# Kernel tuning notes

Hardware: AMD Instinct MI355X
Metric: run time of the kernel (lower is better)

## Reference

```python
import jax, jax.numpy as jnp
import numpy as np

B, C_IN, C_MID, C_OUT, R, K = 2048, 64, 64, 128, 60, 13
EPS = 1e-5


def _gather(x, nei):
    # x: [B, C, 60] -> gather neighbors -> [B, C, 60, 13]
    b, c = x.shape[0], x.shape[1]
    return x[:, :, nei].reshape(b, c, R, K)


def _block(x, nei, g, bta, m, v, W, c):
    # BN (eval mode) -> ReLU -> Conv2d(kernel (1,13)) fused block.
    h = _gather(x, nei)                              # [B,C,60,13]
    inv = g * jax.lax.rsqrt(v + EPS)                 # [C]
    h = jax.nn.relu(h * inv[None, :, None, None] + (bta - m * inv)[None, :, None, None])
    # Conv2d with kernel (1,13), stride 1 == contraction over (c, k)
    return jnp.einsum('bcrk,ock->bor', h, W) + c[None, :, None]  # [B,O,60]


def setup_inputs() -> dict:
    key = jax.random.key(0)
    ks = jax.random.split(key, 24)
    n = lambda k, s: jax.random.normal(k, s, dtype=jnp.float32)
    u = lambda k, s: jax.random.uniform(k, s, dtype=jnp.float32, minval=0.5, maxval=1.5)
    return {
        "x": n(ks[0], (B, C_IN, R)),
        "nei": jax.random.randint(ks[1], (R * K,), 0, R, dtype=jnp.int32),
        # comb_layer_in: BN(in) + Conv(in->mid)
        "g1": n(ks[2], (C_IN,)), "b1": n(ks[3], (C_IN,)), "m1": n(ks[4], (C_IN,)), "v1": u(ks[5], (C_IN,)),
        "W1": n(ks[6], (C_MID, C_IN, K)) * 0.1, "c1": n(ks[7], (C_MID,)) * 0.1,
        # comb_layer_out: BN(mid) + Conv(mid->out)
        "g2": n(ks[8], (C_MID,)), "b2": n(ks[9], (C_MID,)), "m2": n(ks[10], (C_MID,)), "v2": u(ks[11], (C_MID,)),
        "W2": n(ks[12], (C_OUT, C_MID, K)) * 0.1, "c2": n(ks[13], (C_OUT,)) * 0.1,
        # short_cut_layer: BN(in) + Conv(in->out)
        "g3": n(ks[14], (C_IN,)), "b3": n(ks[15], (C_IN,)), "m3": n(ks[16], (C_IN,)), "v3": u(ks[17], (C_IN,)),
        "W3": n(ks[18], (C_OUT, C_IN, K)) * 0.1, "c3": n(ks[19], (C_OUT,)) * 0.1,
    }


def reference(x, nei, g1, b1, m1, v1, W1, c1, g2, b2, m2, v2, W2, c2,
              g3, b3, m3, v3, W3, c3):
    f = _block(x, nei, g1, b1, m1, v1, W1, c1)      # [B, C_MID, 60]
    f = _block(f, nei, g2, b2, m2, v2, W2, c2)      # [B, C_OUT, 60]
    sc = _block(x, nei, g3, b3, m3, v3, W3, c3)     # [B, C_OUT, 60]
    return f + sc
```

## Files before the change

kernel.cpp:

```cpp
#include <hip/hip_runtime.h>
#include <hip/hip_bf16.h>


typedef __attribute__((ext_vector_type(8))) short bf16x8;
typedef __attribute__((ext_vector_type(4))) float f32x4;
typedef __attribute__((ext_vector_type(4))) unsigned short us4;
typedef __attribute__((ext_vector_type(8))) unsigned short us8;

#define EPSV 1e-5f
#define PLANE 131072
#define ZTOT  7864320

__device__ __forceinline__ unsigned short f2bf(float f) {
  unsigned int u = __builtin_bit_cast(unsigned int, f);
  u += 0x7FFFu + ((u >> 16) & 1u);
  return (unsigned short)(u >> 16);
}
__device__ __forceinline__ float bf2f(unsigned short s) {
  unsigned int u = ((unsigned int)s) << 16;
  return __builtin_bit_cast(float, u);
}

typedef const __attribute__((address_space(1))) unsigned int gas_u32;
typedef __attribute__((address_space(3))) unsigned int las_u32;
__device__ __forceinline__ void gl16(const void* g, void* l) {
  __builtin_amdgcn_global_load_lds((gas_u32*)g, (las_u32*)l, 16, 0, 0);
}

__global__ void prep_w(const float* __restrict__ W1, const float* __restrict__ W2,
                       const float* __restrict__ W3,
                       const float* __restrict__ g1, const float* __restrict__ be1,
                       const float* __restrict__ mu1, const float* __restrict__ va1,
                       const float* __restrict__ c1,
                       const float* __restrict__ g2, const float* __restrict__ be2,
                       const float* __restrict__ mu2, const float* __restrict__ va2,
                       const float* __restrict__ c2,
                       const float* __restrict__ g3, const float* __restrict__ be3,
                       const float* __restrict__ mu3, const float* __restrict__ va3,
                       const float* __restrict__ c3,
                       unsigned short* __restrict__ W1t,
                       unsigned short* __restrict__ W23t,
                       float* __restrict__ params) {
  int t = blockIdx.x * 256 + threadIdx.x;
  if (t < 4096) {
    int o = t >> 6, c = t & 63;
    const float* src = W1 + (o * 64 + c) * 13;
    unsigned short* dst = W1t + o * 832 + c;
    #pragma unroll
    for (int ks = 0; ks < 13; ks++) dst[ks * 64] = f2bf(src[ks]);
  } else if (t < 20480) {
    int idx = t - 4096;
    int half = idx >> 13;
    int o = (idx >> 6) & 127, c = idx & 63;
    const float* src = (half ? W3 : W2) + (o * 64 + c) * 13;
    unsigned short* dst = W23t + o * 1664 + half * 13 * 64 + c;
    #pragma unroll
    for (int ks = 0; ks < 13; ks++) dst[ks * 64] = f2bf(src[ks]);
  }
  if (blockIdx.x == 79) {
    int u = threadIdx.x;
    if (u < 64) {
      float a1v = g1[u] * rsqrtf(va1[u] + EPSV);
      params[u]       = a1v;
      params[64 + u]  = be1[u] - mu1[u] * a1v;
      float a3v = g3[u] * rsqrtf(va3[u] + EPSV);
      params[128 + u] = a3v;
      params[192 + u] = be3[u] - mu3[u] * a3v;
      float a2v = g2[u] * rsqrtf(va2[u] + EPSV);
      params[256 + u] = a2v;
      params[320 + u] = be2[u] - mu2[u] * a2v + a2v * c1[u];
    }
    if (u < 128) params[384 + u] = c2[u] + c3[u];
  }
}

__global__ __launch_bounds__(256) void t_in(const float* __restrict__ x,
                                            const float* __restrict__ params,
                                            unsigned short* __restrict__ z1T,
                                            unsigned short* __restrict__ z3T) {
  __shared__ float xt[64 * 61];
  __shared__ float prm[256];
  const int b = blockIdx.x, t = threadIdx.x;
  prm[t] = params[t];
  for (int i = t; i < 3840; i += 256) {
    int c = i / 60;
    xt[c * 61 + (i - c * 60)] = x[b * 3840 + i];
  }
  __syncthreads();
  if (t < 240) {
    int r = t >> 2, g = t & 3, c0 = g << 4;
    us8 z1v0, z1v1, z3v0, z3v1;
    #pragma unroll
    for (int j = 0; j < 8; j++) {
      int c = c0 + j;
      float v = xt[c * 61 + r];
      z1v0[j] = f2bf(fmaxf(fmaf(v, prm[c], prm[64 + c]), 0.f));
      z3v0[j] = f2bf(fmaxf(fmaf(v, prm[128 + c], prm[192 + c]), 0.f));
    }
    #pragma unroll
    for (int j = 0; j < 8; j++) {
      int c = c0 + 8 + j;
      float v = xt[c * 61 + r];
      z1v1[j] = f2bf(fmaxf(fmaf(v, prm[c], prm[64 + c]), 0.f));
      z3v1[j] = f2bf(fmaxf(fmaf(v, prm[128 + c], prm[192 + c]), 0.f));
    }
    int idx = (r * 2048 + b) * 64 + c0;
    *(us8*)(z1T + idx) = z1v0;  *(us8*)(z1T + idx + 8) = z1v1;
    *(us8*)(z3T + idx) = z3v0;  *(us8*)(z3T + idx + 8) = z3v1;
  }
}

#define MFMA __builtin_amdgcn_mfma_f32_16x16x32_bf16

__global__ __launch_bounds__(256, 2) void gemm1(const unsigned short* __restrict__ W1t,
                                                const unsigned short* __restrict__ z1T,
                                                const int* __restrict__ nei,
                                                const float* __restrict__ params,
                                                unsigned short* __restrict__ z2T) {
  __shared__ unsigned short As[2][4096];
  __shared__ unsigned short Bs[2][2][8192];

  const int bid = blockIdx.x;
  const int rp = bid >> 4, btile = bid & 15;
  const int b0 = btile << 7;
  const int rA = rp * 2, rB = rA + 1;
  const int t = threadIdx.x, wave = t >> 6, lane = t & 63;
  const int quad = lane >> 4, nl = lane & 15;
  const int rsel = wave >> 1, nhh = wave & 1;

  int pl0[13], pl1[13];
  #pragma unroll
  for (int q = 0; q < 13; q++) { pl0[q] = nei[rA * 13 + q]; pl1[q] = nei[rB * 13 + q]; }

  const int trow = t >> 3, tj = t & 7;
  const int sw8 = ((tj ^ (trow & 7)) << 3);
  const unsigned short* gA = W1t + trow * 832 + tj * 8;
  const unsigned short* gB = z1T + (b0 + trow) * 64 + tj * 8;
  unsigned short* lA = &As[0][trow * 64 + sw8];
  unsigned short* lB0 = &Bs[0][0][trow * 64 + sw8];
  unsigned short* lB1 = &Bs[0][1][trow * 64 + sw8];

  {
    us8 va0 = *(const us8*)(gA);
    us8 va1 = *(const us8*)(gA + 32 * 832);
    const unsigned short* g0 = gB + pl0[0] * PLANE;
    const unsigned short* g1p = gB + pl1[0] * PLANE;
    us8 b00 = *(const us8*)(g0);
    us8 b01 = *(const us8*)(g0 + 2048);
    us8 b02 = *(const us8*)(g0 + 4096);
    us8 b03 = *(const us8*)(g0 + 6144);
    us8 b10 = *(const us8*)(g1p);
    us8 b11 = *(const us8*)(g1p + 2048);
    us8 b12 = *(const us8*)(g1p + 4096);
    us8 b13 = *(const us8*)(g1p + 6144);
    *(us8*)(lA) = va0;  *(us8*)(lA + 2048) = va1;
    *(us8*)(lB0) = b00; *(us8*)(lB0 + 2048) = b01;
    *(us8*)(lB0 + 4096) = b02; *(us8*)(lB0 + 6144) = b03;
    *(us8*)(lB1) = b10; *(us8*)(lB1 + 2048) = b11;
    *(us8*)(lB1 + 4096) = b12; *(us8*)(lB1 + 6144) = b13;
  }
  __syncthreads();

  const int c0 = ((quad ^ (nl & 7)) << 3);
  f32x4 acc[4][4] = {};
  #pragma unroll 1
  for (int kq = 0; kq < 13; kq++) {
    const int bf = kq & 1;
    us8 va0, va1, b00, b01, b02, b03, b10, b11, b12, b13;
    if (kq < 12) {
      const unsigned short* ga = gA + (kq + 1) * 64;
      va0 = *(const us8*)(ga);
      va1 = *(const us8*)(ga + 32 * 832);
      const unsigned short* g0 = gB + pl0[kq + 1] * PLANE;
      const unsigned short* g1p = gB + pl1[kq + 1] * PLANE;
      b00 = *(const us8*)(g0);        b01 = *(const us8*)(g0 + 2048);
      b02 = *(const us8*)(g0 + 4096); b03 = *(const us8*)(g0 + 6144);
      b10 = *(const us8*)(g1p);        b11 = *(const us8*)(g1p + 2048);
      b12 = *(const us8*)(g1p + 4096); b13 = *(const us8*)(g1p + 6144);
    }
    const unsigned short* Ab = &As[bf][nl * 64];
    const unsigned short* Bb = &Bs[bf][rsel][(nhh * 64 + nl) * 64];
    bf16x8 af[4][2], bfr[4][2];
    #pragma unroll
    for (int mt = 0; mt < 4; mt++) {
      af[mt][0] = *(const bf16x8*)(Ab + mt * 1024 + c0);
      af[mt][1] = *(const bf16x8*)(Ab + mt * 1024 + (c0 ^ 32));
    }
    #pragma unroll
    for (int nt = 0; nt < 4; nt++) {
      bfr[nt][0] = *(const bf16x8*)(Bb + nt * 1024 + c0);
      bfr[nt][1] = *(const bf16x8*)(Bb + nt * 1024 + (c0 ^ 32));
    }
    #pragma unroll
    for (int h = 0; h < 2; h++)
      #pragma unroll
      for (int mt = 0; mt < 4; mt++)
        #pragma unroll
        for (int nt = 0; nt < 4; nt++)
          acc[mt][nt] = MFMA(af[mt][h], bfr[nt][h], acc[mt][nt], 0, 0, 0);
    if (kq < 12) {
      unsigned short* la = lA + (bf ^ 1) * 4096;
      unsigned short* l0 = lB0 + (bf ^ 1) * 16384;
      unsigned short* l1 = lB1 + (bf ^ 1) * 16384;
      *(us8*)(la) = va0;  *(us8*)(la + 2048) = va1;
      *(us8*)(l0) = b00; *(us8*)(l0 + 2048) = b01;
      *(us8*)(l0 + 4096) = b02; *(us8*)(l0 + 6144) = b03;
      *(us8*)(l1) = b10; *(us8*)(l1 + 2048) = b11;
      *(us8*)(l1 + 4096) = b12; *(us8*)(l1 + 6144) = b13;
    }
    __syncthreads();
  }

  const int rr = rA + rsel;
  #pragma unroll
  for (int mt = 0; mt < 4; mt++) {
    int ob = mt * 16 + quad * 4;
    f32x4 av = *(const f32x4*)(params + 256 + ob);
    f32x4 bv = *(const f32x4*)(params + 320 + ob);
    #pragma unroll
    for (int nt = 0; nt < 4; nt++) {
      int col = b0 + nhh * 64 + nt * 16 + nl;
      f32x4 a = acc[mt][nt];
      us4 w;
      w.x = f2bf(fmaxf(fmaf(a[0], av[0], bv[0]), 0.f));
      w.y = f2bf(fmaxf(fmaf(a[1], av[1], bv[1]), 0.f));
      w.z = f2bf(fmaxf(fmaf(a[2], av[2], bv[2]), 0.f));
      w.w = f2bf(fmaxf(fmaf(a[3], av[3], bv[3]), 0.f));
      *(us4*)(z2T + (rr * 2048 + col) * 64 + ob) = w;
    }
  }
}

__global__ __launch_bounds__(256, 2) void gemm2(const unsigned short* __restrict__ W23t,
                                                const unsigned short* __restrict__ z2T,
                                                const unsigned short* __restrict__ z3T,
                                                const int* __restrict__ nei,
                                                const float* __restrict__ params,
                                                unsigned short* __restrict__ outT) {
  __shared__ unsigned short As[3][4096];
  __shared__ unsigned short Bs[3][8192];
  __shared__ int sOff[26];

  const int bid = blockIdx.x;
  const int r = bid >> 3, btile = bid & 7;
  const int b0 = btile << 8;
  const int t = threadIdx.x, wv = t >> 6, lane = t & 63;
  const int quad = lane >> 4, nl = lane & 15;
  const int mh = wv >> 1, nh = wv & 1;

  if (t < 26) {
    int idx = t < 13 ? t : t - 13;
    int p = nei[r * 13 + idx];
    sOff[t] = p * (PLANE * 2) + (t < 13 ? 0 : ZTOT * 2);
  }

  const int lr = lane >> 2, lj = lane & 3;
  const int sj = ((lj ^ ((lr >> 1) & 3)) << 4);
  int aoff[2];
  #pragma unroll
  for (int i = 0; i < 2; i++) aoff[i] = (16 * (2 * wv + i) + lr) * 3328 + sj;
  int boff[4];
  #pragma unroll
  for (int i = 0; i < 4; i++) boff[i] = (b0 + 16 * (4 * wv + i) + lr) * 128 + sj;

  const char* gAb = (const char*)W23t;
  const char* z2b = (const char*)z2T;

  __syncthreads();

  {
    const char* gb = z2b + sOff[0];
    #pragma unroll
    for (int i = 0; i < 2; i++) gl16(gAb + aoff[i], &As[0][(2 * wv + i) * 512]);
    #pragma unroll
    for (int i = 0; i < 4; i++) gl16(gb + boff[i], &Bs[0][(4 * wv + i) * 512]);
    #pragma unroll
    for (int i = 0; i < 2; i++) gl16(gAb + 64 + aoff[i], &As[1][(2 * wv + i) * 512]);
    #pragma unroll
    for (int i = 0; i < 4; i++) gl16(gb + 64 + boff[i], &Bs[1][(4 * wv + i) * 512]);
  }
  asm volatile("s_waitcnt vmcnt(6)" ::: "memory");
  __builtin_amdgcn_s_barrier();

  const int rc = ((quad ^ ((nl >> 1) & 3)) << 3);
  const int aro = (mh * 64 + nl) * 32 + rc;
  const int bro = (nh * 128 + nl) * 32 + rc;

  f32x4 acc[4][8] = {};
  int cb = 0, sb = 2;
  #pragma unroll 1
  for (int s = 0; s < 51; s++) {
    const unsigned short* Ab = &As[cb][aro];
    const unsigned short* Bb = &Bs[cb][bro];
    bf16x8 af[4], bfr[8];
    #pragma unroll
    for (int mt = 0; mt < 4; mt++)
      af[mt] = *(const bf16x8*)(Ab + mt * 512);
    #pragma unroll
    for (int nt = 0; nt < 8; nt++)
      bfr[nt] = *(const bf16x8*)(Bb + nt * 512);
    const int kn = s + 2;
    if (kn < 52) {
      const int pn = kn >> 1;
      int off = sOff[pn] + ((kn & 1) << 6);
      const char* ga = gAb + kn * 64;
      const char* gb = z2b + off;
      #pragma unroll
      for (int i = 0; i < 2; i++) gl16(ga + aoff[i], &As[sb][(2 * wv + i) * 512]);
      #pragma unroll
      for (int i = 0; i < 4; i++) gl16(gb + boff[i], &Bs[sb][(4 * wv + i) * 512]);
    }
    __builtin_amdgcn_s_barrier();
    asm volatile("s_waitcnt lgkmcnt(0)" ::: "memory");
    __builtin_amdgcn_sched_barrier(0);
    __builtin_amdgcn_s_setprio(1);
    #pragma unroll
    for (int mt = 0; mt < 4; mt++)
      #pragma unroll
      for (int nt = 0; nt < 8; nt++)
        acc[mt][nt] = MFMA(af[mt], bfr[nt], acc[mt][nt], 0, 0, 0);
    __builtin_amdgcn_s_setprio(0);
    __builtin_amdgcn_sched_barrier(0);
    asm volatile("s_waitcnt vmcnt(6)" ::: "memory");
    __builtin_amdgcn_s_barrier();
    cb = (cb == 2) ? 0 : cb + 1;
    sb = (sb == 2) ? 0 : sb + 1;
  }
  {
    asm volatile("s_waitcnt vmcnt(0)" ::: "memory");
    __builtin_amdgcn_s_barrier();
    const unsigned short* Ab = &As[0][aro];
    const unsigned short* Bb = &Bs[0][bro];
    bf16x8 af[4], bfr[8];
    #pragma unroll
    for (int mt = 0; mt < 4; mt++)
      af[mt] = *(const bf16x8*)(Ab + mt * 512);
    #pragma unroll
    for (int nt = 0; nt < 8; nt++)
      bfr[nt] = *(const bf16x8*)(Bb + nt * 512);
    #pragma unroll
    for (int mt = 0; mt < 4; mt++)
      #pragma unroll
      for (int nt = 0; nt < 8; nt++)
        acc[mt][nt] = MFMA(af[mt], bfr[nt], acc[mt][nt], 0, 0, 0);
  }

  #pragma unroll
  for (int mt = 0; mt < 4; mt++) {
    int ob = mh * 64 + mt * 16 + quad * 4;
    f32x4 cv = *(const f32x4*)(params + 384 + ob);
    #pragma unroll
    for (int nt = 0; nt < 8; nt++) {
      int col = b0 + nh * 128 + nt * 16 + nl;
      f32x4 a = acc[mt][nt];
      us4 w;
      w.x = f2bf(a[0] + cv[0]);
      w.y = f2bf(a[1] + cv[1]);
      w.z = f2bf(a[2] + cv[2]);
      w.w = f2bf(a[3] + cv[3]);
      *(us4*)(outT + (r * 2048 + col) * 128 + ob) = w;
    }
  }
}

__global__ __launch_bounds__(256) void t_out(const unsigned short* __restrict__ outT,
                                             float* __restrict__ out) {
  __shared__ float ot[60 * 129];
  const int b = blockIdx.x, t = threadIdx.x;
  for (int i = t; i < 1920; i += 256) {
    int r = i >> 5, og = (i & 31) << 2;
    us4 v = *(const us4*)(outT + (r * 2048 + b) * 128 + og);
    ot[r * 129 + og + 0] = bf2f(v.x);
    ot[r * 129 + og + 1] = bf2f(v.y);
    ot[r * 129 + og + 2] = bf2f(v.z);
    ot[r * 129 + og + 3] = bf2f(v.w);
  }
  __syncthreads();
  int o = t >> 1, s = t & 1;
  float* dst = out + b * 7680 + o * 60 + s * 30;
  #pragma unroll
  for (int j = 0; j < 30; j++) dst[j] = ot[(s * 30 + j) * 129 + o];
}

extern "C" void kernel_launch(void* const* d_in, const int* in_sizes, int n_in,
                              void* d_out, int out_size, void* d_ws, size_t ws_size,
                              hipStream_t stream) {
  const float* x   = (const float*)d_in[0];
  const int*   nei = (const int*)d_in[1];
  const float* g1  = (const float*)d_in[2];
  const float* be1 = (const float*)d_in[3];
  const float* mu1 = (const float*)d_in[4];
  const float* va1 = (const float*)d_in[5];
  const float* W1  = (const float*)d_in[6];
  const float* c1  = (const float*)d_in[7];
  const float* g2  = (const float*)d_in[8];
  const float* be2 = (const float*)d_in[9];
  const float* mu2 = (const float*)d_in[10];
  const float* va2 = (const float*)d_in[11];
  const float* W2  = (const float*)d_in[12];
  const float* c2  = (const float*)d_in[13];
  const float* g3  = (const float*)d_in[14];
  const float* be3 = (const float*)d_in[15];
  const float* mu3 = (const float*)d_in[16];
  const float* va3 = (const float*)d_in[17];
  const float* W3  = (const float*)d_in[18];
  const float* c3  = (const float*)d_in[19];

  unsigned short* W1t  = (unsigned short*)d_ws;
  unsigned short* W23t = W1t + 53248;
  float*          prm  = (float*)(W23t + 212992);
  unsigned short* z2T  = (unsigned short*)(prm + 512);
  unsigned short* z3T  = z2T + ZTOT;
  unsigned short* big  = z3T + ZTOT;
  unsigned short* z1T  = big;
  unsigned short* outT = big;

  prep_w<<<80, 256, 0, stream>>>(W1, W2, W3,
                                 g1, be1, mu1, va1, c1,
                                 g2, be2, mu2, va2, c2,
                                 g3, be3, mu3, va3, c3,
                                 W1t, W23t, prm);
  t_in<<<2048, 256, 0, stream>>>(x, prm, z1T, z3T);
  gemm1<<<480, 256, 0, stream>>>(W1t, z1T, nei, prm, z2T);
  gemm2<<<480, 256, 0, stream>>>(W23t, z2T, z3T, nei, prm, outT);
  t_out<<<2048, 256, 0, stream>>>(outT, (float*)d_out);
}
```

Baseline: 235.4 us.

## Rework gemm1 with direct global-to-LDS loads, triple buffering, one row per block

gemm1 now handles one output row and a 256-column batch tile per block instead of two rows and 128 columns. It streams 32-wide K slices through a three-stage LDS ring filled by direct global-to-LDS loads (gl16), coordinated by explicit vmcnt waits, barriers and MFMA priority boosts. The intent is to overlap global gathers with MFMA work and drop the register staging through VGPRs. t_out's final store is also rewritten so consecutive threads write consecutive addresses, giving coalesced output writes at the cost of an integer divide per element.

```diff
diff --git a/kernel.cpp b/kernel.cpp
--- a/kernel.cpp
+++ b/kernel.cpp
@@ -117,101 +117,104 @@
                                                 const int* __restrict__ nei,
                                                 const float* __restrict__ params,
                                                 unsigned short* __restrict__ z2T) {
-  __shared__ unsigned short As[2][4096];
-  __shared__ unsigned short Bs[2][2][8192];
+  __shared__ unsigned short As[3][2048];
+  __shared__ unsigned short Bs[3][8192];
+  __shared__ int sOff[13];
 
   const int bid = blockIdx.x;
-  const int rp = bid >> 4, btile = bid & 15;
-  const int b0 = btile << 7;
-  const int rA = rp * 2, rB = rA + 1;
-  const int t = threadIdx.x, wave = t >> 6, lane = t & 63;
+  const int r = bid >> 3, btile = bid & 7;
+  const int b0 = btile << 8;
+  const int t = threadIdx.x, wv = t >> 6, lane = t & 63;
   const int quad = lane >> 4, nl = lane & 15;
-  const int rsel = wave >> 1, nhh = wave & 1;
-
-  int pl0[13], pl1[13];
+
+  if (t < 13) sOff[t] = nei[r * 13 + t] * (PLANE * 2);
+
+  const int lr = lane >> 2, lj = lane & 3;
+  const int sj = ((lj ^ ((lr >> 1) & 3)) << 4);
+  const int aoff = (16 * wv + lr) * 1664 + sj;
+  int boff[4];
   #pragma unroll
-  for (int q = 0; q < 13; q++) { pl0[q] = nei[rA * 13 + q]; pl1[q] = nei[rB * 13 + q]; }
-
-  const int trow = t >> 3, tj = t & 7;
-  const int sw8 = ((tj ^ (trow & 7)) << 3);
-  const unsigned short* gA = W1t + trow * 832 + tj * 8;
-  const unsigned short* gB = z1T + (b0 + trow) * 64 + tj * 8;
-  unsigned short* lA = &As[0][trow * 64 + sw8];
-  unsigned short* lB0 = &Bs[0][0][trow * 64 + sw8];
-  unsigned short* lB1 = &Bs[0][1][trow * 64 + sw8];
+  for (int i = 0; i < 4; i++) boff[i] = (b0 + 16 * (4 * wv + i) + lr) * 128 + sj;
+
+  const char* gAb = (const char*)W1t;
+  const char* z1b = (const char*)z1T;
+
+  __syncthreads();
 
   {
-    us8 va0 = *(const us8*)(gA);
-    us8 va1 = *(const us8*)(gA + 32 * 832);
-    const unsigned short* g0 = gB + pl0[0] * PLANE;
-    const unsigned short* g1p = gB + pl1[0] * PLANE;
-    us8 b00 = *(const us8*)(g0);
-    us8 b01 = *(const us8*)(g0 + 2048);
-    us8 b02 = *(const us8*)(g0 + 4096);
-    us8 b03 = *(const us8*)(g0 + 6144);
-    us8 b10 = *(const us8*)(g1p);
-    us8 b11 = *(const us8*)(g1p + 2048);
-    us8 b12 = *(const us8*)(g1p + 4096);
-    us8 b13 = *(const us8*)(g1p + 6144);
-    *(us8*)(lA) = va0;  *(us8*)(lA + 2048) = va1;
-    *(us8*)(lB0) = b00; *(us8*)(lB0 + 2048) = b01;
-    *(us8*)(lB0 + 4096) = b02; *(us8*)(lB0 + 6144) = b03;
-    *(us8*)(lB1) = b10; *(us8*)(lB1 + 2048) = b11;
-    *(us8*)(lB1 + 4096) = b12; *(us8*)(lB1 + 6144) = b13;
-  }
-  __syncthreads();
-
-  const int c0 = ((quad ^ (nl & 7)) << 3);
+    const char* gb = z1b + sOff[0];
+    gl16(gAb + aoff, &As[0][wv * 512]);
+    #pragma unroll
+    for (int i = 0; i < 4; i++) gl16(gb + boff[i], &Bs[0][(4 * wv + i) * 512]);
+    gl16(gAb + 64 + aoff, &As[1][wv * 512]);
+    #pragma unroll
+    for (int i = 0; i < 4; i++) gl16(gb + 64 + boff[i], &Bs[1][(4 * wv + i) * 512]);
+  }
+  asm volatile("s_waitcnt vmcnt(5)" ::: "memory");
+  __builtin_amdgcn_s_barrier();
+
+  const int rc = ((quad ^ ((nl >> 1) & 3)) << 3);
+  const int aro = nl * 32 + rc;
+  const int bro = (wv * 64 + nl) * 32 + rc;
+
   f32x4 acc[4][4] = {};
+  int cb = 0, sb = 2;
   #pragma unroll 1
-  for (int kq = 0; kq < 13; kq++) {
-    const int bf = kq & 1;
-    us8 va0, va1, b00, b01, b02, b03, b10, b11, b12, b13;
-    if (kq < 12) {
-      const unsigned short* ga = gA + (kq + 1) * 64;
-      va0 = *(const us8*)(ga);
-      va1 = *(const us8*)(ga + 32 * 832);
-      const unsigned short* g0 = gB + pl0[kq + 1] * PLANE;
-      const unsigned short* g1p = gB + pl1[kq + 1] * PLANE;
-      b00 = *(const us8*)(g0);        b01 = *(const us8*)(g0 + 2048);
-      b02 = *(const us8*)(g0 + 4096); b03 = *(const us8*)(g0 + 6144);
-      b10 = *(const us8*)(g1p);        b11 = *(const us8*)(g1p + 2048);
-      b12 = *(const us8*)(g1p + 4096); b13 = *(const us8*)(g1p + 6144);
-    }
-    const unsigned short* Ab = &As[bf][nl * 64];
-    const unsigned short* Bb = &Bs[bf][rsel][(nhh * 64 + nl) * 64];
-    bf16x8 af[4][2], bfr[4][2];
-    #pragma unroll
-    for (int mt = 0; mt < 4; mt++) {
-      af[mt][0] = *(const bf16x8*)(Ab + mt * 1024 + c0);
-      af[mt][1] = *(const bf16x8*)(Ab + mt * 1024 + (c0 ^ 32));
-    }
-    #pragma unroll
-    for (int nt = 0; nt < 4; nt++) {
-      bfr[nt][0] = *(const bf16x8*)(Bb + nt * 1024 + c0);
-      bfr[nt][1] = *(const bf16x8*)(Bb + nt * 1024 + (c0 ^ 32));
-    }
-    #pragma unroll
-    for (int h = 0; h < 2; h++)
-      #pragma unroll
-      for (int mt = 0; mt < 4; mt++)
-        #pragma unroll
-        for (int nt = 0; nt < 4; nt++)
-          acc[mt][nt] = MFMA(af[mt][h], bfr[nt][h], acc[mt][nt], 0, 0, 0);
-    if (kq < 12) {
-      unsigned short* la = lA + (bf ^ 1) * 4096;
-      unsigned short* l0 = lB0 + (bf ^ 1) * 16384;
-      unsigned short* l1 = lB1 + (bf ^ 1) * 16384;
-      *(us8*)(la) = va0;  *(us8*)(la + 2048) = va1;
-      *(us8*)(l0) = b00; *(us8*)(l0 + 2048) = b01;
-      *(us8*)(l0 + 4096) = b02; *(us8*)(l0 + 6144) = b03;
-      *(us8*)(l1) = b10; *(us8*)(l1 + 2048) = b11;
-      *(us8*)(l1 + 4096) = b12; *(us8*)(l1 + 6144) = b13;
-    }
-    __syncthreads();
-  }
-
-  const int rr = rA + rsel;
+  for (int s = 0; s < 25; s++) {
+    const unsigned short* Ab = &As[cb][aro];
+    const unsigned short* Bb = &Bs[cb][bro];
+    bf16x8 af[4], bfr[4];
+    #pragma unroll
+    for (int mt = 0; mt < 4; mt++)
+      af[mt] = *(const bf16x8*)(Ab + mt * 512);
+    #pragma unroll
+    for (int nt = 0; nt < 4; nt++)
+      bfr[nt] = *(const bf16x8*)(Bb + nt * 512);
+    const int kn = s + 2;
+    if (kn < 26) {
+      const int pn = kn >> 1;
+      int off = sOff[pn] + ((kn & 1) << 6);
+      const char* ga = gAb + kn * 64;
+      const char* gb = z1b + off;
+      gl16(ga + aoff, &As[sb][wv * 512]);
+      #pragma unroll
+      for (int i = 0; i < 4; i++) gl16(gb + boff[i], &Bs[sb][(4 * wv + i) * 512]);
+    }
+    __builtin_amdgcn_s_barrier();
+    asm volatile("s_waitcnt lgkmcnt(0)" ::: "memory");
+    __builtin_amdgcn_sched_barrier(0);
+    __builtin_amdgcn_s_setprio(1);
+    #pragma unroll
+    for (int mt = 0; mt < 4; mt++)
+      #pragma unroll
+      for (int nt = 0; nt < 4; nt++)
+        acc[mt][nt] = MFMA(af[mt], bfr[nt], acc[mt][nt], 0, 0, 0);
+    __builtin_amdgcn_s_setprio(0);
+    __builtin_amdgcn_sched_barrier(0);
+    asm volatile("s_waitcnt vmcnt(5)" ::: "memory");
+    __builtin_amdgcn_s_barrier();
+    cb = (cb == 2) ? 0 : cb + 1;
+    sb = (sb == 2) ? 0 : sb + 1;
+  }
+  {
+    asm volatile("s_waitcnt vmcnt(0)" ::: "memory");
+    __builtin_amdgcn_s_barrier();
+    const unsigned short* Ab = &As[1][aro];
+    const unsigned short* Bb = &Bs[1][bro];
+    bf16x8 af[4], bfr[4];
+    #pragma unroll
+    for (int mt = 0; mt < 4; mt++)
+      af[mt] = *(const bf16x8*)(Ab + mt * 512);
+    #pragma unroll
+    for (int nt = 0; nt < 4; nt++)
+      bfr[nt] = *(const bf16x8*)(Bb + nt * 512);
+    #pragma unroll
+    for (int mt = 0; mt < 4; mt++)
+      #pragma unroll
+      for (int nt = 0; nt < 4; nt++)
+        acc[mt][nt] = MFMA(af[mt], bfr[nt], acc[mt][nt], 0, 0, 0);
+  }
+
   #pragma unroll
   for (int mt = 0; mt < 4; mt++) {
     int ob = mt * 16 + quad * 4;
@@ -219,14 +222,14 @@
     f32x4 bv = *(const f32x4*)(params + 320 + ob);
     #pragma unroll
     for (int nt = 0; nt < 4; nt++) {
-      int col = b0 + nhh * 64 + nt * 16 + nl;
+      int col = b0 + wv * 64 + nt * 16 + nl;
       f32x4 a = acc[mt][nt];
       us4 w;
       w.x = f2bf(fmaxf(fmaf(a[0], av[0], bv[0]), 0.f));
       w.y = f2bf(fmaxf(fmaf(a[1], av[1], bv[1]), 0.f));
       w.z = f2bf(fmaxf(fmaf(a[2], av[2], bv[2]), 0.f));
       w.w = f2bf(fmaxf(fmaf(a[3], av[3], bv[3]), 0.f));
-      *(us4*)(z2T + (rr * 2048 + col) * 64 + ob) = w;
+      *(us4*)(z2T + (r * 2048 + col) * 64 + ob) = w;
     }
   }
 }
@@ -376,10 +379,11 @@
     ot[r * 129 + og + 3] = bf2f(v.w);
   }
   __syncthreads();
-  int o = t >> 1, s = t & 1;
-  float* dst = out + b * 7680 + o * 60 + s * 30;
-  #pragma unroll
-  for (int j = 0; j < 30; j++) dst[j] = ot[(s * 30 + j) * 129 + o];
+  float* dst = out + b * 7680;
+  for (int i = t; i < 7680; i += 256) {
+    int o = i / 60, r = i - o * 60;
+    dst[i] = ot[r * 129 + o];
+  }
 }
 
 extern "C" void kernel_launch(void* const* d_in, const int* in_sizes, int n_in,
```

New measurement: 224.2 us. -4.7%, faster.
